# Kernel optimization log

Measured on AMD Instinct MI355X. Metric: run time of the kernel, lower is better.

Reference implementation:

```python
import jax, jax.numpy as jnp
import numpy as np

# Mamba2 config (from init_kwargs + mamba_ssm Mamba2 defaults)
D_MODEL = 256
D_STATE = 16
D_CONV = 4
EXPAND = 2
HEADDIM = 64                      # Mamba2 default
D_INNER = EXPAND * D_MODEL        # 512
NHEADS = D_INNER // HEADDIM       # 8
CONV_DIM = D_INNER + 2 * D_STATE  # 544 (ngroups=1)
D_IN_PROJ = 2 * D_INNER + 2 * D_STATE + NHEADS  # 1064
B, H, W = 8, 64, 64
EPS = 1e-5


def setup_inputs() -> dict:
    key = jax.random.key(0)
    ks = jax.random.split(key, 8)
    x = jax.random.normal(ks[0], (B, D_MODEL, H, W), jnp.float32)
    ln_w = jnp.ones((D_MODEL,), jnp.float32)
    ln_b = jnp.zeros((D_MODEL,), jnp.float32)
    in_proj_w = jax.random.normal(ks[1], (D_IN_PROJ, D_MODEL), jnp.float32) * (D_MODEL ** -0.5)
    conv_w = jax.random.normal(ks[2], (CONV_DIM, D_CONV), jnp.float32) * (D_CONV ** -0.5)
    conv_b = jnp.zeros((CONV_DIM,), jnp.float32)
    dt = jax.random.uniform(ks[3], (NHEADS,), jnp.float32, 1e-3, 0.1)
    dt_bias = dt + jnp.log(-jnp.expm1(-dt))  # inverse softplus
    A_log = jnp.log(jax.random.uniform(ks[4], (NHEADS,), jnp.float32, 1.0, 16.0))
    D = jnp.ones((NHEADS,), jnp.float32)
    rms_w = jnp.ones((D_INNER,), jnp.float32)
    out_proj_w = jax.random.normal(ks[5], (D_MODEL, D_INNER), jnp.float32) * (D_INNER ** -0.5)
    return dict(x=x, ln_w=ln_w, ln_b=ln_b, in_proj_w=in_proj_w, conv_w=conv_w,
                conv_b=conv_b, dt_bias=dt_bias, A_log=A_log, D=D, rms_w=rms_w,
                out_proj_w=out_proj_w)


def reference(x, ln_w, ln_b, in_proj_w, conv_w, conv_b, dt_bias, A_log, D, rms_w, out_proj_w):
    Bb, C, Hh, Ww = x.shape
    L = Hh * Ww
    # (B,C,H,W) -> (B,L,C)
    xs = x.transpose(0, 2, 3, 1).reshape(Bb, L, C)
    # pre-LayerNorm
    mu = jnp.mean(xs, -1, keepdims=True)
    var = jnp.mean((xs - mu) ** 2, -1, keepdims=True)
    xn = (xs - mu) * jax.lax.rsqrt(var + EPS) * ln_w + ln_b
    # input projection -> z | xBC | dt
    zxbcdt = xn @ in_proj_w.T
    z = zxbcdt[..., :D_INNER]
    xBC = zxbcdt[..., D_INNER:D_INNER + CONV_DIM]
    dt = jax.nn.softplus(zxbcdt[..., D_INNER + CONV_DIM:] + dt_bias)  # (B,L,NH)
    # causal depthwise conv1d (kernel D_CONV) + SiLU
    xp = jnp.pad(xBC, ((0, 0), (D_CONV - 1, 0), (0, 0)))
    conv = conv_b
    for k in range(D_CONV):  # small fixed kernel loop
        conv = conv + xp[:, k:k + L, :] * conv_w[:, k]
    xBC = jax.nn.silu(conv)
    xh = xBC[..., :D_INNER].reshape(Bb, L, NHEADS, HEADDIM)
    Bm = xBC[..., D_INNER:D_INNER + D_STATE]   # (B,L,N)
    Cm = xBC[..., D_INNER + D_STATE:]          # (B,L,N)
    A = -jnp.exp(A_log)                        # (NH,)
    dA = jnp.exp(dt * A)                       # (B,L,NH)
    dtx = dt[..., None] * xh                   # (B,L,NH,P)

    def step(h, inp):
        dA_t, dtx_t, B_t, C_t = inp
        # h: (B,NH,P,N)
        h = dA_t[:, :, None, None] * h + dtx_t[..., None] * B_t[:, None, None, :]
        y = jnp.einsum('bhpn,bn->bhp', h, C_t)
        return h, y

    h0 = jnp.zeros((Bb, NHEADS, HEADDIM, D_STATE), xs.dtype)
    _, ys = jax.lax.scan(step, h0, (dA.transpose(1, 0, 2), dtx.transpose(1, 0, 2, 3),
                                    Bm.transpose(1, 0, 2), Cm.transpose(1, 0, 2)))
    y = ys.transpose(1, 0, 2, 3) + D[:, None] * xh   # (B,L,NH,P)
    y = y.reshape(Bb, L, D_INNER)
    # gated RMSNorm (norm_before_gate=False): rmsnorm(y * silu(z)) * w
    y = y * jax.nn.silu(z)
    y = y * jax.lax.rsqrt(jnp.mean(y * y, -1, keepdims=True) + EPS) * rms_w
    out = y @ out_proj_w.T
    out = out.reshape(Bb, Hh, Ww, C).transpose(0, 3, 1, 2) + x
    return out
```

## Files before the change

kernel.cpp:

```cpp
#include <hip/hip_runtime.h>
#include <cstdint>

typedef unsigned short u16;
typedef unsigned int u32;
typedef u16 u16x8 __attribute__((ext_vector_type(8)));
typedef u16 u16x4 __attribute__((ext_vector_type(4)));
typedef short short8 __attribute__((ext_vector_type(8)));
typedef float f32x4 __attribute__((ext_vector_type(4)));

__device__ __forceinline__ float bf2f(u16 u){ return __uint_as_float(((u32)u)<<16); }
__device__ __forceinline__ u16 f2bf(float f){
  u32 x = __float_as_uint(f);
  return (u16)((x + 0x7fffu + ((x>>16)&1u)) >> 16);
}
__device__ __forceinline__ float siluf(float v){ return v/(1.f + __expf(-v)); }


__global__ __launch_bounds__(256) void k0_wprep(const float* __restrict__ w1,
                                                const float* __restrict__ w2,
                                                u16* __restrict__ w1b, u16* __restrict__ w2b){
  u32 idx = blockIdx.x*256u + threadIdx.x;
  const u32 W1N = 1152u*256u;
  const u32 W2N = 256u*512u;
  if (idx < W1N){
    u32 n = idx >> 8;
    w1b[idx] = (n < 1064u) ? f2bf(w1[idx]) : (u16)0;
  } else if (idx < W1N + W2N){
    u32 j = idx - W1N;
    w2b[j] = f2bf(w2[j]);
  }
}

__global__ __launch_bounds__(256) void k1_ln(const float* __restrict__ x,
                                             const float* __restrict__ ln_w, const float* __restrict__ ln_b,
                                             const float* __restrict__ w1,
                                             u16* __restrict__ xnb, float* __restrict__ dtr){
  __shared__ float tile[256][33];
  __shared__ float mu_s[32], rs_s[32];
  const int b  = blockIdx.y;
  const int l0 = blockIdx.x*32;
  const int tid = threadIdx.x;
  const size_t xbase = (size_t)b*256*4096;
  const int cl = tid>>5;
  const int ll = tid&31;
  for (int cc=0; cc<256; cc+=8){
    int c = cc + cl;
    tile[c][ll] = x[xbase + (size_t)c*4096 + l0 + ll];
  }
  __syncthreads();
  const int lane = tid&63, wave = tid>>6;
  const int lidx = wave*8 + (lane&7);
  const int c0 = (lane>>3)*32;
  float s=0.f, ss=0.f;
  for (int c=c0; c<c0+32; ++c){ float v = tile[c][lidx]; s += v; ss += v*v; }
  for (int off=8; off<64; off<<=1){ s += __shfl_xor(s, off); ss += __shfl_xor(ss, off); }
  float mu = s*(1.f/256.f);
  float var = ss*(1.f/256.f) - mu*mu;
  float rs = rsqrtf(var + 1e-5f);
  if ((lane>>3)==0){ mu_s[lidx]=mu; rs_s[lidx]=rs; }
  __syncthreads();
  {
    const int c = tid;
    const float lw = ln_w[c], lb = ln_b[c];
    for (int l=0; l<32; ++l){
      float v = (tile[c][l]-mu_s[l])*rs_s[l]*lw + lb;
      xnb[((size_t)b*4096 + l0 + l)*256 + c] = f2bf(v);
    }
  }
  {
    const int r = tid>>3, j = tid&7;
    const float* wr = w1 + (size_t)(1056+j)*256;
    const float mur = mu_s[r], rsr = rs_s[r];
    float acc = 0.f;
    for (int c=0; c<256; ++c){
      float v = (tile[c][r]-mur)*rsr*ln_w[c] + ln_b[c];
      acc += v*wr[c];
    }
    dtr[((size_t)b*4096 + l0 + r)*8 + j] = acc;
  }
}

__global__ __launch_bounds__(256) void k2_gemm1(const u16* __restrict__ A, const u16* __restrict__ W,
                                                u16* __restrict__ zb, u16* __restrict__ xT){
  __shared__ u16 sA[128*40];
  __shared__ u16 sW[128*40];
  const int tid = threadIdx.x, lane = tid&63, wave = tid>>6;
  const int s = blockIdx.x;
  const int kx = s & 7;
  const int idx = s >> 3;
  const int xn = idx % 9;
  const int ym = (idx/9)*8 + kx;
  const size_t m0 = (size_t)ym*128;
  const int n0 = xn*128;
  const int wm = (wave>>1)*64, wn = (wave&1)*64;
  f32x4 acc[4][4] = {};
  const int fr = lane&15, kc = (lane>>4)*8;
  for (int k0=0; k0<256; k0+=32){
    #pragma unroll
    for (int j=0; j<2; ++j){
      int ch = j*256 + tid, r = ch>>2, co = (ch&3)*8;
      *(u16x8*)&sA[r*40+co] = *(const u16x8*)&A[(m0+r)*256 + k0 + co];
      *(u16x8*)&sW[r*40+co] = *(const u16x8*)&W[(size_t)(n0+r)*256 + k0 + co];
    }
    __syncthreads();
    short8 af[4], bf4[4];
    #pragma unroll
    for (int fm=0; fm<4; ++fm) af[fm]  = *(short8*)&sA[(wm+fm*16+fr)*40 + kc];
    #pragma unroll
    for (int fn=0; fn<4; ++fn) bf4[fn] = *(short8*)&sW[(wn+fn*16+fr)*40 + kc];
    #pragma unroll
    for (int fm=0; fm<4; ++fm)
      #pragma unroll
      for (int fn=0; fn<4; ++fn)
        acc[fm][fn] = __builtin_amdgcn_mfma_f32_16x16x32_bf16(af[fm],bf4[fn],acc[fm][fn],0,0,0);
    __syncthreads();
  }
  #pragma unroll
  for (int fm=0; fm<4; ++fm)
    #pragma unroll
    for (int fn=0; fn<4; ++fn){
      int rb = wm + fm*16 + ((lane>>4)<<2);
      int col = n0 + wn + fn*16 + (lane&15);
      size_t m = m0 + rb;
      if (col < 512){
        #pragma unroll
        for (int i=0; i<4; ++i) zb[(m+i)*512 + col] = f2bf(acc[fm][fn][i]);
      } else if (col < 1056){
        u16x4 o;
        #pragma unroll
        for (int i=0; i<4; ++i) o[i] = f2bf(acc[fm][fn][i]);
        *(u16x4*)&xT[(size_t)(col-512)*32768 + m] = o;
      }
    }
}

__global__ __launch_bounds__(256,3) void kU(const u16* __restrict__ xT, const float* __restrict__ dtr,
                                          const float* __restrict__ conv_w, const float* __restrict__ conv_b,
                                          const float* __restrict__ dt_bias, const float* __restrict__ A_log,
                                          float* __restrict__ hend, float* __restrict__ aprod){
  __shared__ char lds[44816];
  float* rawB = (float*)(lds + 0);
  u16*   BcT  = (u16*)(lds + 4560);
  float* wl   = (float*)(lds + 6864);
  const int ck = blockIdx.x, b = blockIdx.y, half = blockIdx.z;
  const int tid = threadIdx.x, lane = tid&63, hh = tid>>6;
  const int h = half*4 + hh;
  const int m0 = b*4096 + ck*64;
  u16* XW = (u16*)(lds + 7888 + hh*9232);
  for (int i=tid; i<16*72; i+=256){
    int n = i/72, r = i - n*72;
    if (r < 67){
      int l = ck*64 - 3 + r;
      rawB[r*17+n] = (l>=0) ? bf2f(xT[(size_t)(512+n)*32768 + (size_t)b*4096 + l]) : 0.f;
    }
  }
  {
    int t = lane;
    float dr = dtr[(size_t)(m0+t)*8 + h] + dt_bias[h];
    float dt = (dr > 20.f) ? dr : log1pf(__expf(dr));
    float Ah = -__expf(A_log[h]);
    float v = dt*Ah;
    #pragma unroll
    for (int off=1; off<64; off<<=1){ float p = __shfl_up(v, off); if (lane >= off) v += p; }
    float scT = __shfl(v, 63);
    wl[hh*64 + t] = dt * __expf(scT - v);
    if (lane==0) aprod[(b*8+h)*64 + ck] = __expf(scT);
  }
  __syncthreads();
  for (int i=tid; i<16*64; i+=256){
    int n = i>>6, s2 = i&63;
    int c = 512+n;
    float a = conv_b[c] + conv_w[c*4+0]*rawB[s2*17+n] + conv_w[c*4+1]*rawB[(s2+1)*17+n]
            + conv_w[c*4+2]*rawB[(s2+2)*17+n] + conv_w[c*4+3]*rawB[(s2+3)*17+n];
    BcT[n*72 + s2] = f2bf(siluf(a));
  }
  {
    const int c = h*64 + lane;
    const float w0=conv_w[c*4], w1=conv_w[c*4+1], w2=conv_w[c*4+2], w3=conv_w[c*4+3];
    const float cb = conv_b[c];
    const u16* xcol = xT + (size_t)c*32768 + (size_t)b*4096 + ck*64;
    u16x8 wv[9]; u16x8 zer = {};
    wv[0] = (ck>0) ? *(const u16x8*)(xcol - 8) : zer;
    #pragma unroll
    for (int j=0;j<8;++j) wv[j+1] = *(const u16x8*)(xcol + j*8);
    #pragma unroll
    for (int t8=0; t8<8; ++t8){
      u16x8 o;
      #pragma unroll
      for (int j=0;j<8;++j){
        const int t = t8*8+j;
        float x0 = bf2f(wv[(t+5)>>3][(t+5)&7]);
        float x1 = bf2f(wv[(t+6)>>3][(t+6)&7]);
        float x2 = bf2f(wv[(t+7)>>3][(t+7)&7]);
        float x3 = bf2f(wv[(t+8)>>3][(t+8)&7]);
        o[j] = f2bf(siluf(cb + w0*x0 + w1*x1 + w2*x2 + w3*x3) * wl[hh*64 + t]);
      }
      *(u16x8*)&XW[lane*72 + t8*8] = o;
    }
  }
  __syncthreads();
  const int fr = lane&15, g = lane>>4;
  f32x4 acc4[4] = {};
  #pragma unroll
  for (int ks=0; ks<2; ++ks){
    short8 bfr = *(short8*)&BcT[fr*72 + ks*32 + g*8];
    #pragma unroll
    for (int ti=0; ti<4; ++ti){
      short8 afr = *(short8*)&XW[(ti*16+fr)*72 + ks*32 + g*8];
      acc4[ti] = __builtin_amdgcn_mfma_f32_16x16x32_bf16(afr, bfr, acc4[ti], 0,0,0);
    }
  }
  size_t hb = ((size_t)((b*8+h)*64 + ck))*64;
  #pragma unroll
  for (int ti=0; ti<4; ++ti)
    #pragma unroll
    for (int i=0; i<4; ++i){
      int p = ti*16 + g*4 + i;
      hend[(hb + p)*16 + fr] = acc4[ti][i];
    }
}

__global__ __launch_bounds__(64) void k5_phase2(const float* __restrict__ hend, const float* __restrict__ aprod,
                                                float* __restrict__ hs){
  const int bh = blockIdx.x;
  const int lane = threadIdx.x;
  float hr[16];
  #pragma unroll
  for (int n=0;n<16;++n) hr[n]=0.f;
  for (int ck=0; ck<64; ++ck){
    size_t base = (((size_t)bh*64 + ck)*64 + lane)*16;
    float a = aprod[bh*64 + ck];
    #pragma unroll
    for (int n=0;n<16;++n) hs[base+n] = hr[n];
    #pragma unroll
    for (int n=0;n<16;++n) hr[n] = a*hr[n] + hend[base+n];
  }
}

__global__ __launch_bounds__(256,3) void kY(const u16* __restrict__ xT, const float* __restrict__ dtr,
                                          const float* __restrict__ conv_w, const float* __restrict__ conv_b,
                                          const float* __restrict__ dt_bias, const float* __restrict__ A_log,
                                          const float* __restrict__ Dp, const float* __restrict__ hs,
                                          u16* __restrict__ ybh){
  __shared__ char lds[52416];
  u16*   G     = (u16*)(lds + 0);
  float* rawBC = (float*)(lds + 0);
  u16*   Cc    = (u16*)(lds + 9216);
  u16*   Bc    = (u16*)(lds + 11264);
  float* scs   = (float*)(lds + 13312);
  float* dth   = (float*)(lds + 14400);
  const int ck = blockIdx.x, b = blockIdx.y, half = blockIdx.z;
  const int tid = threadIdx.x, lane = tid&63, hh = tid>>6;
  const int h = half*4 + hh;
  const int m0 = b*4096 + ck*64;
  u16* XT = (u16*)(lds + 15488 + hh*9232);
  for (int i=tid; i<32*72; i+=256){
    int n = i/72, r = i - n*72;
    if (r < 67){
      int l = ck*64 - 3 + r;
      rawBC[r*33+n] = (l>=0) ? bf2f(xT[(size_t)(512+n)*32768 + (size_t)b*4096 + l]) : 0.f;
    }
  }
  {
    int t = lane;
    float dr = dtr[(size_t)(m0+t)*8 + h] + dt_bias[h];
    float dt = (dr > 20.f) ? dr : log1pf(__expf(dr));
    float Ah = -__expf(A_log[h]);
    float v = dt*Ah;
    #pragma unroll
    for (int off=1; off<64; off<<=1){ float p = __shfl_up(v, off); if (lane >= off) v += p; }
    dth[hh*68 + t] = dt;
    scs[hh*68 + t] = v;
  }
  {
    const int c = h*64 + lane;
    const float w0=conv_w[c*4], w1=conv_w[c*4+1], w2=conv_w[c*4+2], w3=conv_w[c*4+3];
    const float cb = conv_b[c];
    const u16* xcol = xT + (size_t)c*32768 + (size_t)b*4096 + ck*64;
    u16x8 wv[9]; u16x8 zer = {};
    wv[0] = (ck>0) ? *(const u16x8*)(xcol - 8) : zer;
    #pragma unroll
    for (int j=0;j<8;++j) wv[j+1] = *(const u16x8*)(xcol + j*8);
    #pragma unroll
    for (int t8=0; t8<8; ++t8){
      u16x8 o;
      #pragma unroll
      for (int j=0;j<8;++j){
        const int t = t8*8+j;
        float x0 = bf2f(wv[(t+5)>>3][(t+5)&7]);
        float x1 = bf2f(wv[(t+6)>>3][(t+6)&7]);
        float x2 = bf2f(wv[(t+7)>>3][(t+7)&7]);
        float x3 = bf2f(wv[(t+8)>>3][(t+8)&7]);
        o[j] = f2bf(siluf(cb + w0*x0 + w1*x1 + w2*x2 + w3*x3));
      }
      *(u16x8*)&XT[lane*72 + t8*8] = o;
    }
  }
  __syncthreads();
  for (int i=tid; i<64*32; i+=256){
    int s2 = i>>5, n = i&31;
    int c = 512 + n;
    float a = conv_b[c] + conv_w[c*4+0]*rawBC[s2*33+n] + conv_w[c*4+1]*rawBC[(s2+1)*33+n]
            + conv_w[c*4+2]*rawBC[(s2+2)*33+n] + conv_w[c*4+3]*rawBC[(s2+3)*33+n];
    u16 v = f2bf(siluf(a));
    if (n < 16) Bc[s2*16 + n] = v; else Cc[s2*16 + (n-16)] = v;
  }
  __syncthreads();
  const int fr = lane&15, g = lane>>4;
  #define GFRAG(TI,SJ) { \
    short8 ca = {}, bb = {}; \
    if (g < 2){ ca = *(short8*)&Cc[((TI)*16+fr)*16 + g*8]; bb = *(short8*)&Bc[((SJ)*16+fr)*16 + g*8]; } \
    f32x4 d = {}; \
    d = __builtin_amdgcn_mfma_f32_16x16x32_bf16(ca,bb,d,0,0,0); \
    G[((TI)*16 + g*4 + 0)*72 + (SJ)*16 + fr] = f2bf(d[0]); \
    G[((TI)*16 + g*4 + 1)*72 + (SJ)*16 + fr] = f2bf(d[1]); \
    G[((TI)*16 + g*4 + 2)*72 + (SJ)*16 + fr] = f2bf(d[2]); \
    G[((TI)*16 + g*4 + 3)*72 + (SJ)*16 + fr] = f2bf(d[3]); }
  if      (hh==0){ GFRAG(0,0) GFRAG(2,1) GFRAG(3,2) }
  else if (hh==1){ GFRAG(1,0) GFRAG(2,2) GFRAG(3,3) }
  else if (hh==2){ GFRAG(1,1) GFRAG(3,0) }
  else           { GFRAG(2,0) GFRAG(3,1) }
  #undef GFRAG
  __syncthreads();
  f32x4 acc[4][4] = {};
  {
    size_t hsbase = ((size_t)((b*8+h)*64 + ck))*64*16;
    short8 h0f[4];
    #pragma unroll
    for (int pj=0; pj<4; ++pj){
      short8 hf = {};
      if (g < 2){
        int p = pj*16 + fr;
        f32x4 lo = *(const f32x4*)&hs[hsbase + p*16 + g*8];
        f32x4 hi = *(const f32x4*)&hs[hsbase + p*16 + g*8 + 4];
        #pragma unroll
        for (int kk=0; kk<4; ++kk){ hf[kk] = (short)f2bf(lo[kk]); hf[kk+4] = (short)f2bf(hi[kk]); }
      }
      h0f[pj] = hf;
    }
    #pragma unroll
    for (int ti=0; ti<4; ++ti){
      short8 ca = {};
      if (g < 2) ca = *(short8*)&Cc[(ti*16+fr)*16 + g*8];
      #pragma unroll
      for (int pj=0; pj<4; ++pj)
        acc[ti][pj] = __builtin_amdgcn_mfma_f32_16x16x32_bf16(ca, h0f[pj], acc[ti][pj], 0,0,0);
    }
  }
  #pragma unroll
  for (int ti=0; ti<4; ++ti)
    #pragma unroll
    for (int i=0; i<4; ++i){
      float pt = __expf(scs[hh*68 + ti*16 + g*4 + i]);
      #pragma unroll
      for (int pj=0; pj<4; ++pj) acc[ti][pj][i] *= pt;
    }
  #pragma unroll
  for (int ks=0; ks<2; ++ks){
    short8 xf[4];
    #pragma unroll
    for (int pj=0; pj<4; ++pj) xf[pj] = *(short8*)&XT[(pj*16+fr)*72 + ks*32 + g*8];
    #pragma unroll
    for (int ti=0; ti<4; ++ti){
      if (ks*32 > ti*16+15) continue;
      int t = ti*16 + fr;
      float sct = scs[hh*68 + t];
      f32x4 sc0 = *(f32x4*)&scs[hh*68 + ks*32 + g*8];
      f32x4 sc1 = *(f32x4*)&scs[hh*68 + ks*32 + g*8 + 4];
      f32x4 dt0 = *(f32x4*)&dth[hh*68 + ks*32 + g*8];
      f32x4 dt1 = *(f32x4*)&dth[hh*68 + ks*32 + g*8 + 4];
      u16x8 g8 = *(u16x8*)&G[t*72 + ks*32 + g*8];
      short8 mf;
      #pragma unroll
      for (int kk=0; kk<8; ++kk){
        int s2 = ks*32 + g*8 + kk;
        float sv = (kk<4) ? sc0[kk] : sc1[kk-4];
        float dv = (kk<4) ? dt0[kk] : dt1[kk-4];
        float m = (s2 <= t) ? bf2f(g8[kk]) * __expf(sct - sv) * dv : 0.f;
        mf[kk] = (short)f2bf(m);
      }
      #pragma unroll
      for (int pj=0; pj<4; ++pj)
        acc[ti][pj] = __builtin_amdgcn_mfma_f32_16x16x32_bf16(mf, xf[pj], acc[ti][pj], 0,0,0);
    }
  }
  {
    const float Dh = Dp[h];
    #pragma unroll
    for (int ti=0; ti<4; ++ti)
      #pragma unroll
      for (int pj=0; pj<4; ++pj){
        int p = pj*16 + fr;
        u16x4 xv = *(u16x4*)&XT[p*72 + ti*16 + g*4];
        #pragma unroll
        for (int i=0; i<4; ++i) acc[ti][pj][i] += Dh * bf2f(xv[i]);
      }
  }
  #pragma unroll
  for (int ti=0; ti<4; ++ti)
    #pragma unroll
    for (int pj=0; pj<4; ++pj)
      #pragma unroll
      for (int i=0; i<4; ++i)
        XT[(ti*16 + g*4 + i)*72 + pj*16 + fr] = f2bf(acc[ti][pj][i]);
  __syncthreads();
  {
    const int hl = lane>>4;
    const u16* R = (const u16*)(lds + 15488 + hl*9232);
    #pragma unroll
    for (int tt=0; tt<16; ++tt){
      int t = hh*16 + tt;
      u16x4 v = *(const u16x4*)&R[t*72 + (lane&15)*4];
      *(u16x4*)&ybh[(size_t)(m0+t)*512 + half*256 + lane*4] = v;
    }
  }
}

__global__ __launch_bounds__(256) void k7_rms(const u16* __restrict__ y, const u16* __restrict__ zb,
                                              const float* __restrict__ rms_w, u16* __restrict__ ynb){
  const int m = blockIdx.x*4 + (threadIdx.x>>6);
  const int lane = threadIdx.x&63;
  const size_t base = (size_t)m*512 + lane*8;
  u16x8 yv = *(const u16x8*)&y[base];
  u16x8 zv = *(const u16x8*)&zb[base];
  float g[8];
  float ssum = 0.f;
  #pragma unroll
  for (int j=0;j<8;++j){
    float zf = bf2f(zv[j]);
    float sig = 1.f/(1.f + __expf(-zf));
    g[j] = bf2f(yv[j]) * (zf*sig);
    ssum += g[j]*g[j];
  }
  for (int off=1; off<64; off<<=1) ssum += __shfl_xor(ssum, off);
  float rs = rsqrtf(ssum*(1.f/512.f) + 1e-5f);
  u16x8 o;
  #pragma unroll
  for (int j=0;j<8;++j) o[j] = f2bf(g[j]*rs*rms_w[lane*8+j]);
  *(u16x8*)&ynb[base] = o;
}

__global__ __launch_bounds__(256) void k8_gemm2(const u16* __restrict__ A, const u16* __restrict__ W,
                                                const float* __restrict__ xres, float* __restrict__ out){
  __shared__ float smem[4*64*65];
  u16* sA = (u16*)smem;
  u16* sW = ((u16*)smem) + 128*40;
  const int tid = threadIdx.x, lane = tid&63, wave = tid>>6;
  const int s = blockIdx.x;
  const int kx = s & 7;
  const int idx = s >> 3;
  const int xn = idx & 1;
  const int ym = (idx>>1)*8 + kx;
  const size_t m0 = (size_t)ym*128;
  const int n0 = xn*128;
  const int wm = (wave>>1)*64, wn = (wave&1)*64;
  f32x4 acc[4][4] = {};
  const int fr = lane&15, kc = (lane>>4)*8;
  for (int k0=0; k0<512; k0+=32){
    #pragma unroll
    for (int j=0; j<2; ++j){
      int ch = j*256 + tid, r = ch>>2, co = (ch&3)*8;
      *(u16x8*)&sA[r*40+co] = *(const u16x8*)&A[(m0+r)*512 + k0 + co];
      *(u16x8*)&sW[r*40+co] = *(const u16x8*)&W[(size_t)(n0+r)*512 + k0 + co];
    }
    __syncthreads();
    short8 af[4], bf4[4];
    #pragma unroll
    for (int fm=0; fm<4; ++fm) af[fm]  = *(short8*)&sA[(wm+fm*16+fr)*40 + kc];
    #pragma unroll
    for (int fn=0; fn<4; ++fn) bf4[fn] = *(short8*)&sW[(wn+fn*16+fr)*40 + kc];
    #pragma unroll
    for (int fm=0; fm<4; ++fm)
      #pragma unroll
      for (int fn=0; fn<4; ++fn)
        acc[fm][fn] = __builtin_amdgcn_mfma_f32_16x16x32_bf16(af[fm],bf4[fn],acc[fm][fn],0,0,0);
    __syncthreads();
  }
  float* T = smem + wave*(64*65);
  #pragma unroll
  for (int fm=0; fm<4; ++fm)
    #pragma unroll
    for (int fn=0; fn<4; ++fn){
      int rr = fm*16 + ((lane>>4)<<2);
      int cc = fn*16 + (lane&15);
      #pragma unroll
      for (int i=0; i<4; ++i) T[(rr+i)*65 + cc] = acc[fm][fn][i];
    }
  __syncthreads();
  const int bb = (int)(m0>>12);
  const int lbase = (int)(m0&4095) + wm;
  for (int cc=0; cc<64; ++cc){
    int col = n0 + wn + cc;
    size_t o = ((size_t)bb*256 + col)*4096 + lbase + lane;
    out[o] = T[lane*65 + cc] + xres[o];
  }
}

extern "C" void kernel_launch(void* const* d_in, const int* in_sizes, int n_in,
                              void* d_out, int out_size, void* d_ws, size_t ws_size,
                              hipStream_t stream){
  const float* x        = (const float*)d_in[0];
  const float* ln_w     = (const float*)d_in[1];
  const float* ln_b     = (const float*)d_in[2];
  const float* in_proj  = (const float*)d_in[3];
  const float* conv_w   = (const float*)d_in[4];
  const float* conv_b   = (const float*)d_in[5];
  const float* dt_bias  = (const float*)d_in[6];
  const float* A_log    = (const float*)d_in[7];
  const float* Dp       = (const float*)d_in[8];
  const float* rms_w    = (const float*)d_in[9];
  const float* out_proj = (const float*)d_in[10];
  float* out = (float*)d_out;

  char* ws = (char*)d_ws;
  const size_t o_w1   = 0;
  const size_t o_w2   = 589824;
  const size_t o_xn   = 851968;
  const size_t o_z    = 17629184;
  const size_t o_xT   = 51183616;
  const size_t o_dtr  = 86835200;
  const size_t o_hend = 87883776;
  const size_t o_hs   = 104660992;
  const size_t o_ap   = 121438208;
  const size_t o_ybh  = 121454592;
  const size_t NEED   = 155009024;
  if (ws_size < NEED) return;

  u16*   w1b  = (u16*)(ws + o_w1);
  u16*   w2b  = (u16*)(ws + o_w2);
  u16*   xnb  = (u16*)(ws + o_xn);
  u16*   zbuf = (u16*)(ws + o_z);
  u16*   xTb  = (u16*)(ws + o_xT);
  float* dtr  = (float*)(ws + o_dtr);
  float* hend = (float*)(ws + o_hend);
  float* hsb  = (float*)(ws + o_hs);
  float* ap   = (float*)(ws + o_ap);
  u16*   ybh  = (u16*)(ws + o_ybh);
  u16*   ynb  = (u16*)(ws + o_hend);

  k0_wprep<<<1664, 256, 0, stream>>>(in_proj, out_proj, w1b, w2b);
  k1_ln<<<dim3(128, 8), 256, 0, stream>>>(x, ln_w, ln_b, in_proj, xnb, dtr);
  k2_gemm1<<<2304, 256, 0, stream>>>(xnb, w1b, zbuf, xTb);
  kU<<<dim3(64, 8, 2), 256, 0, stream>>>(xTb, dtr, conv_w, conv_b, dt_bias, A_log, hend, ap);
  k5_phase2<<<64, 64, 0, stream>>>(hend, ap, hsb);
  kY<<<dim3(64, 8, 2), 256, 0, stream>>>(xTb, dtr, conv_w, conv_b, dt_bias, A_log, Dp, hsb, ybh);
  k7_rms<<<8192, 256, 0, stream>>>(ybh, zbuf, rms_w, ynb);
  k8_gemm2<<<512, 256, 0, stream>>>(ynb, w2b, x, out);
}
```

Measured before the change: 284.9 us.

## Fuse gated RMSNorm into SSM output kernel and store z transposed

The chunk-output kernel now runs all 8 heads in one 512-thread block, so each block holds the full 512-wide row and applies the SiLU gate and RMSNorm before writing. This removes the separate RMS kernel and the round trip of the y buffer through memory. GEMM1 now writes z in the same transposed layout as xBC, and the phase-2 scan is split across 4 waves that each use vectorised float4 loads and stores. The cost is that z is now read with a stride of 32768 elements per element, which makes those reads uncoalesced, and the larger LDS footprint lowers occupancy.

```diff
diff --git a/kernel.cpp b/kernel.cpp
--- a/kernel.cpp
+++ b/kernel.cpp
@@ -81,7 +81,7 @@
 }
 
 __global__ __launch_bounds__(256) void k2_gemm1(const u16* __restrict__ A, const u16* __restrict__ W,
-                                                u16* __restrict__ zb, u16* __restrict__ xT){
+                                                u16* __restrict__ zxT){
   __shared__ u16 sA[128*40];
   __shared__ u16 sW[128*40];
   const int tid = threadIdx.x, lane = tid&63, wave = tid>>6;
@@ -122,14 +122,11 @@
       int rb = wm + fm*16 + ((lane>>4)<<2);
       int col = n0 + wn + fn*16 + (lane&15);
       size_t m = m0 + rb;
-      if (col < 512){
-        #pragma unroll
-        for (int i=0; i<4; ++i) zb[(m+i)*512 + col] = f2bf(acc[fm][fn][i]);
-      } else if (col < 1056){
+      if (col < 1056){
         u16x4 o;
         #pragma unroll
         for (int i=0; i<4; ++i) o[i] = f2bf(acc[fm][fn][i]);
-        *(u16x4*)&xT[(size_t)(col-512)*32768 + m] = o;
+        *(u16x4*)&zxT[(size_t)col*32768 + m] = o;
       }
     }
 }
@@ -220,41 +217,39 @@
     }
 }
 
-__global__ __launch_bounds__(64) void k5_phase2(const float* __restrict__ hend, const float* __restrict__ aprod,
-                                                float* __restrict__ hs){
+__global__ __launch_bounds__(256) void k5_phase2(const float* __restrict__ hend, const float* __restrict__ aprod,
+                                                 float* __restrict__ hs){
   const int bh = blockIdx.x;
-  const int lane = threadIdx.x;
-  float hr[16];
-  #pragma unroll
-  for (int n=0;n<16;++n) hr[n]=0.f;
+  const int w = threadIdx.x>>6, lane = threadIdx.x&63;
+  const int n0 = w*4;
+  f32x4 hr = {0.f,0.f,0.f,0.f};
   for (int ck=0; ck<64; ++ck){
-    size_t base = (((size_t)bh*64 + ck)*64 + lane)*16;
+    size_t base = (((size_t)bh*64 + ck)*64 + lane)*16 + n0;
     float a = aprod[bh*64 + ck];
-    #pragma unroll
-    for (int n=0;n<16;++n) hs[base+n] = hr[n];
-    #pragma unroll
-    for (int n=0;n<16;++n) hr[n] = a*hr[n] + hend[base+n];
-  }
-}
-
-__global__ __launch_bounds__(256,3) void kY(const u16* __restrict__ xT, const float* __restrict__ dtr,
-                                          const float* __restrict__ conv_w, const float* __restrict__ conv_b,
-                                          const float* __restrict__ dt_bias, const float* __restrict__ A_log,
-                                          const float* __restrict__ Dp, const float* __restrict__ hs,
-                                          u16* __restrict__ ybh){
-  __shared__ char lds[52416];
+    *(f32x4*)&hs[base] = hr;
+    f32x4 he = *(const f32x4*)&hend[base];
+    hr = a*hr + he;
+  }
+}
+
+__global__ __launch_bounds__(512) void kYR(const u16* __restrict__ xT, const u16* __restrict__ zxT,
+                                           const float* __restrict__ dtr,
+                                           const float* __restrict__ conv_w, const float* __restrict__ conv_b,
+                                           const float* __restrict__ dt_bias, const float* __restrict__ A_log,
+                                           const float* __restrict__ Dp, const float* __restrict__ rms_w,
+                                           const float* __restrict__ hs, u16* __restrict__ ynb){
+  __shared__ char lds[91520];
   u16*   G     = (u16*)(lds + 0);
   float* rawBC = (float*)(lds + 0);
   u16*   Cc    = (u16*)(lds + 9216);
   u16*   Bc    = (u16*)(lds + 11264);
   float* scs   = (float*)(lds + 13312);
-  float* dth   = (float*)(lds + 14400);
-  const int ck = blockIdx.x, b = blockIdx.y, half = blockIdx.z;
+  float* dth   = (float*)(lds + 15488);
+  const int ck = blockIdx.x, b = blockIdx.y;
   const int tid = threadIdx.x, lane = tid&63, hh = tid>>6;
-  const int h = half*4 + hh;
   const int m0 = b*4096 + ck*64;
-  u16* XT = (u16*)(lds + 15488 + hh*9232);
-  for (int i=tid; i<32*72; i+=256){
+  u16* XT = (u16*)(lds + 17664 + hh*9232);
+  for (int i=tid; i<32*72; i+=512){
     int n = i/72, r = i - n*72;
     if (r < 67){
       int l = ck*64 - 3 + r;
@@ -263,9 +258,9 @@
   }
   {
     int t = lane;
-    float dr = dtr[(size_t)(m0+t)*8 + h] + dt_bias[h];
+    float dr = dtr[(size_t)(m0+t)*8 + hh] + dt_bias[hh];
     float dt = (dr > 20.f) ? dr : log1pf(__expf(dr));
-    float Ah = -__expf(A_log[h]);
+    float Ah = -__expf(A_log[hh]);
     float v = dt*Ah;
     #pragma unroll
     for (int off=1; off<64; off<<=1){ float p = __shfl_up(v, off); if (lane >= off) v += p; }
@@ -273,7 +268,7 @@
     scs[hh*68 + t] = v;
   }
   {
-    const int c = h*64 + lane;
+    const int c = hh*64 + lane;
     const float w0=conv_w[c*4], w1=conv_w[c*4+1], w2=conv_w[c*4+2], w3=conv_w[c*4+3];
     const float cb = conv_b[c];
     const u16* xcol = xT + (size_t)c*32768 + (size_t)b*4096 + ck*64;
@@ -297,7 +292,7 @@
     }
   }
   __syncthreads();
-  for (int i=tid; i<64*32; i+=256){
+  for (int i=tid; i<64*32; i+=512){
     int s2 = i>>5, n = i&31;
     int c = 512 + n;
     float a = conv_b[c] + conv_w[c*4+0]*rawBC[s2*33+n] + conv_w[c*4+1]*rawBC[(s2+1)*33+n]
@@ -316,15 +311,19 @@
     G[((TI)*16 + g*4 + 1)*72 + (SJ)*16 + fr] = f2bf(d[1]); \
     G[((TI)*16 + g*4 + 2)*72 + (SJ)*16 + fr] = f2bf(d[2]); \
     G[((TI)*16 + g*4 + 3)*72 + (SJ)*16 + fr] = f2bf(d[3]); }
-  if      (hh==0){ GFRAG(0,0) GFRAG(2,1) GFRAG(3,2) }
-  else if (hh==1){ GFRAG(1,0) GFRAG(2,2) GFRAG(3,3) }
-  else if (hh==2){ GFRAG(1,1) GFRAG(3,0) }
-  else           { GFRAG(2,0) GFRAG(3,1) }
+  if      (hh==0){ GFRAG(0,0) GFRAG(3,2) }
+  else if (hh==1){ GFRAG(1,0) GFRAG(3,3) }
+  else if (hh==2){ GFRAG(1,1) }
+  else if (hh==3){ GFRAG(2,0) }
+  else if (hh==4){ GFRAG(2,1) }
+  else if (hh==5){ GFRAG(2,2) }
+  else if (hh==6){ GFRAG(3,0) }
+  else           { GFRAG(3,1) }
   #undef GFRAG
   __syncthreads();
   f32x4 acc[4][4] = {};
   {
-    size_t hsbase = ((size_t)((b*8+h)*64 + ck))*64*16;
+    size_t hsbase = ((size_t)((b*8+hh)*64 + ck))*64*16;
     short8 h0f[4];
     #pragma unroll
     for (int pj=0; pj<4; ++pj){
@@ -385,7 +384,7 @@
     }
   }
   {
-    const float Dh = Dp[h];
+    const float Dh = Dp[hh];
     #pragma unroll
     for (int ti=0; ti<4; ++ti)
       #pragma unroll
@@ -405,39 +404,41 @@
         XT[(ti*16 + g*4 + i)*72 + pj*16 + fr] = f2bf(acc[ti][pj][i]);
   __syncthreads();
   {
-    const int hl = lane>>4;
-    const u16* R = (const u16*)(lds + 15488 + hl*9232);
-    #pragma unroll
-    for (int tt=0; tt<16; ++tt){
-      int t = hh*16 + tt;
-      u16x4 v = *(const u16x4*)&R[t*72 + (lane&15)*4];
-      *(u16x4*)&ybh[(size_t)(m0+t)*512 + half*256 + lane*4] = v;
-    }
-  }
-}
-
-__global__ __launch_bounds__(256) void k7_rms(const u16* __restrict__ y, const u16* __restrict__ zb,
-                                              const float* __restrict__ rms_w, u16* __restrict__ ynb){
-  const int m = blockIdx.x*4 + (threadIdx.x>>6);
-  const int lane = threadIdx.x&63;
-  const size_t base = (size_t)m*512 + lane*8;
-  u16x8 yv = *(const u16x8*)&y[base];
-  u16x8 zv = *(const u16x8*)&zb[base];
-  float g[8];
-  float ssum = 0.f;
-  #pragma unroll
-  for (int j=0;j<8;++j){
-    float zf = bf2f(zv[j]);
-    float sig = 1.f/(1.f + __expf(-zf));
-    g[j] = bf2f(yv[j]) * (zf*sig);
-    ssum += g[j]*g[j];
-  }
-  for (int off=1; off<64; off<<=1) ssum += __shfl_xor(ssum, off);
-  float rs = rsqrtf(ssum*(1.f/512.f) + 1e-5f);
-  u16x8 o;
-  #pragma unroll
-  for (int j=0;j<8;++j) o[j] = f2bf(g[j]*rs*rms_w[lane*8+j]);
-  *(u16x8*)&ynb[base] = o;
+    const int r = tid>>3;
+    const int q = tid&7;
+    u16* Yq = (u16*)(lds + 17664 + q*9232);
+    const size_t mrow = (size_t)m0 + r;
+    float ssum = 0.f;
+    #pragma unroll
+    for (int jv=0; jv<8; ++jv){
+      u16x8 yv = *(u16x8*)&Yq[r*72 + jv*8];
+      u16x8 gv;
+      #pragma unroll
+      for (int j=0; j<8; ++j){
+        int p = q*64 + jv*8 + j;
+        float zf = bf2f(zxT[(size_t)p*32768 + mrow]);
+        float gg = bf2f(yv[j]) * (zf/(1.f + __expf(-zf)));
+        ssum += gg*gg;
+        gv[j] = f2bf(gg);
+      }
+      *(u16x8*)&Yq[r*72 + jv*8] = gv;
+    }
+    ssum += __shfl_xor(ssum, 1);
+    ssum += __shfl_xor(ssum, 2);
+    ssum += __shfl_xor(ssum, 4);
+    float rs = rsqrtf(ssum*(1.f/512.f) + 1e-5f);
+    #pragma unroll
+    for (int jv=0; jv<8; ++jv){
+      u16x8 gv = *(u16x8*)&Yq[r*72 + jv*8];
+      u16x8 o;
+      #pragma unroll
+      for (int j=0; j<8; ++j){
+        int p = q*64 + jv*8 + j;
+        o[j] = f2bf(bf2f(gv[j]) * rs * rms_w[p]);
+      }
+      *(u16x8*)&ynb[mrow*512 + q*64 + jv*8] = o;
+    }
+  }
 }
 
 __global__ __launch_bounds__(256) void k8_gemm2(const u16* __restrict__ A, const u16* __restrict__ W,
@@ -516,34 +517,31 @@
   const size_t o_w1   = 0;
   const size_t o_w2   = 589824;
   const size_t o_xn   = 851968;
-  const size_t o_z    = 17629184;
-  const size_t o_xT   = 51183616;
+  const size_t o_zxT  = 17629184;
   const size_t o_dtr  = 86835200;
   const size_t o_hend = 87883776;
   const size_t o_hs   = 104660992;
   const size_t o_ap   = 121438208;
-  const size_t o_ybh  = 121454592;
+  const size_t o_ynb  = 121454592;
   const size_t NEED   = 155009024;
   if (ws_size < NEED) return;
 
   u16*   w1b  = (u16*)(ws + o_w1);
   u16*   w2b  = (u16*)(ws + o_w2);
   u16*   xnb  = (u16*)(ws + o_xn);
-  u16*   zbuf = (u16*)(ws + o_z);
-  u16*   xTb  = (u16*)(ws + o_xT);
+  u16*   zxT  = (u16*)(ws + o_zxT);
+  u16*   xTb  = zxT + (size_t)512*32768;
   float* dtr  = (float*)(ws + o_dtr);
   float* hend = (float*)(ws + o_hend);
   float* hsb  = (float*)(ws + o_hs);
   float* ap   = (float*)(ws + o_ap);
-  u16*   ybh  = (u16*)(ws + o_ybh);
-  u16*   ynb  = (u16*)(ws + o_hend);
+  u16*   ynb  = (u16*)(ws + o_ynb);
 
   k0_wprep<<<1664, 256, 0, stream>>>(in_proj, out_proj, w1b, w2b);
   k1_ln<<<dim3(128, 8), 256, 0, stream>>>(x, ln_w, ln_b, in_proj, xnb, dtr);
-  k2_gemm1<<<2304, 256, 0, stream>>>(xnb, w1b, zbuf, xTb);
+  k2_gemm1<<<2304, 256, 0, stream>>>(xnb, w1b, zxT);
   kU<<<dim3(64, 8, 2), 256, 0, stream>>>(xTb, dtr, conv_w, conv_b, dt_bias, A_log, hend, ap);
-  k5_phase2<<<64, 64, 0, stream>>>(hend, ap, hsb);
-  kY<<<dim3(64, 8, 2), 256, 0, stream>>>(xTb, dtr, conv_w, conv_b, dt_bias, A_log, Dp, hsb, ybh);
-  k7_rms<<<8192, 256, 0, stream>>>(ybh, zbuf, rms_w, ynb);
+  k5_phase2<<<64, 256, 0, stream>>>(hend, ap, hsb);
+  kYR<<<dim3(64, 8), 512, 0, stream>>>(xTb, zxT, dtr, conv_w, conv_b, dt_bias, A_log, Dp, rms_w, hsb, ynb);
   k8_gemm2<<<512, 256, 0, stream>>>(ynb, w2b, x, out);
 }
```

After: 303.6 us. 6.6% more time.
